# Performance work log

Hardware: AMD Instinct MI355X
Metric: run time of the kernel (lower is better)

Reference implementation:

```python
import jax, jax.numpy as jnp
import numpy as np

N_NODES = 50000
N_EDGES = 800000
D_IN = 128
D_OUT = 128


def setup_inputs() -> dict:
    key = jax.random.key(0)
    k1, k2, k3, k4, k5 = jax.random.split(key, 5)
    x = jax.random.normal(k1, (N_NODES, D_IN), dtype=jnp.float32)
    # fc weight, torch Linear convention: [out_dim, in_dim]
    W = jax.random.normal(k2, (D_OUT, D_IN), dtype=jnp.float32) * (1.0 / np.sqrt(D_IN))
    # attn_fc weight: [1, 2*out_dim], no bias
    a = jax.random.normal(k3, (1, 2 * D_OUT), dtype=jnp.float32) * (1.0 / np.sqrt(2 * D_OUT))
    src = jax.random.randint(k4, (N_EDGES,), 0, N_NODES)
    dst = jax.random.randint(k5, (N_EDGES,), 0, N_NODES)
    return {"x": x, "W": W, "a": a, "src": src, "dst": dst}


def reference(x, W, a, src, dst):
    # h = fc(x)
    h = x @ W.T  # [N, D_OUT]
    # attn_fc(cat([h_src, h_dst])) == h_src @ a[:D] + h_dst @ a[D:] (linear, no bias),
    # so precompute per-node scalars instead of materializing [E, 2*D_OUT].
    a_src = a[0, :D_OUT]
    a_dst = a[0, D_OUT:]
    s = h @ a_src  # [N]
    d = h @ a_dst  # [N]
    e = jax.nn.sigmoid(s[src] + d[dst])[:, None]  # [E, 1]
    msg = e * h[src]  # [E, D_OUT]  edge gather + weight
    # reduce: f[v] = sum over incoming edges of e * h_src
    f = jax.ops.segment_sum(msg, dst, num_segments=N_NODES)  # [N, D_OUT]
    return f
```

## Files before the change

kernel.cpp:

```cpp
#include <hip/hip_runtime.h>
#include <hip/hip_bf16.h>
#include <stdint.h>

#define NN 50000
#define NE 800000
#define DD 128
#define NBKT 782
#define BCH 4096
#define BGRID ((NE + BCH - 1) / BCH)
#define CAP 1280
#define SPILL_CAP 32768
#define GROWS 32
#define GGRID ((NN + GROWS - 1) / GROWS)

typedef __attribute__((ext_vector_type(8))) unsigned short ushort8;
typedef __attribute__((ext_vector_type(8))) short short8;
typedef __attribute__((ext_vector_type(4))) float f32x4;

__device__ inline uint16_t f2bf(float f) {
    uint32_t u = __float_as_uint(f);
    return (uint16_t)((u + 0x7fffu + ((u >> 16) & 1u)) >> 16);
}
__device__ inline float bf_lo(uint32_t u) { return __uint_as_float(u << 16); }
__device__ inline float bf_hi(uint32_t u) { return __uint_as_float(u & 0xffff0000u); }

__global__ __launch_bounds__(256) void wconv_k(const float* __restrict__ W,
                                               uint16_t* __restrict__ Wb,
                                               int* __restrict__ cntg) {
    int t = threadIdx.x;
    if (blockIdx.x == 0) {
        for (int k = t; k < NBKT + 4; k += 256) cntg[k] = 0;
    }
    int i = blockIdx.x * 256 + t;
    if (i < DD * DD) Wb[i] = f2bf(W[i]);
}

__global__ __launch_bounds__(256) void gemm_mfma_k(const float* __restrict__ x,
                                                   const uint16_t* __restrict__ Wb,
                                                   const float* __restrict__ a,
                                                   uint16_t* __restrict__ hb,
                                                   float* __restrict__ sArr,
                                                   float* __restrict__ dArr) {
    __shared__ __align__(16) uint16_t hs[GROWS][136];
    __shared__ float sdl[2 * GROWS];
    const int t = threadIdx.x, l = t & 63, wid = t >> 6;
    const int r0 = blockIdx.x * GROWS;
    const int wr0 = (wid >> 1) * 16;
    const int wc0 = (wid & 1) * 64;
    const int lr = l & 15, lk = l >> 4;
    if (t < 2 * GROWS) sdl[t] = 0.f;
    __syncthreads();

    f32x4 acc[4] = {{0.f,0.f,0.f,0.f},{0.f,0.f,0.f,0.f},{0.f,0.f,0.f,0.f},{0.f,0.f,0.f,0.f}};
    const int arow = r0 + wr0 + lr;
    const bool rok = arow < NN;
    const float* xp = x + (size_t)arow * DD + lk * 8;

    #pragma unroll
    for (int kc = 0; kc < 4; ++kc) {
        short8 af;
        if (rok) {
            float4 v0 = *(const float4*)(xp + kc * 32);
            float4 v1 = *(const float4*)(xp + kc * 32 + 4);
            af[0] = (short)f2bf(v0.x); af[1] = (short)f2bf(v0.y);
            af[2] = (short)f2bf(v0.z); af[3] = (short)f2bf(v0.w);
            af[4] = (short)f2bf(v1.x); af[5] = (short)f2bf(v1.y);
            af[6] = (short)f2bf(v1.z); af[7] = (short)f2bf(v1.w);
        } else {
            af = short8{0,0,0,0,0,0,0,0};
        }
        #pragma unroll
        for (int c = 0; c < 4; ++c) {
            int col = wc0 + c * 16 + lr;
            short8 bf_ = *(const short8*)(Wb + (size_t)col * DD + kc * 32 + lk * 8);
            acc[c] = __builtin_amdgcn_mfma_f32_16x16x32_bf16(af, bf_, acc[c], 0, 0, 0);
        }
    }

    float avs[4], avd[4];
    #pragma unroll
    for (int c = 0; c < 4; ++c) {
        avs[c] = a[wc0 + c * 16 + lr];
        avd[c] = a[DD + wc0 + c * 16 + lr];
    }
    #pragma unroll
    for (int i = 0; i < 4; ++i) {
        float ps = 0.f, pd = 0.f;
        #pragma unroll
        for (int c = 0; c < 4; ++c) {
            ps = fmaf(acc[c][i], avs[c], ps);
            pd = fmaf(acc[c][i], avd[c], pd);
        }
        #pragma unroll
        for (int o = 8; o > 0; o >>= 1) {
            ps += __shfl_xor(ps, o);
            pd += __shfl_xor(pd, o);
        }
        if (lr == 0) {
            int brow = wr0 + lk * 4 + i;
            atomicAdd(&sdl[brow], ps);
            atomicAdd(&sdl[GROWS + brow], pd);
        }
    }
    #pragma unroll
    for (int c = 0; c < 4; ++c)
        #pragma unroll
        for (int i = 0; i < 4; ++i)
            hs[wr0 + lk * 4 + i][wc0 + c * 16 + lr] = f2bf(acc[c][i]);
    __syncthreads();

    {
        int row = t >> 3, colg = (t & 7) * 16;
        int grow = r0 + row;
        if (grow < NN) {
            ushort8 v0 = *(const ushort8*)&hs[row][colg];
            ushort8 v1 = *(const ushort8*)&hs[row][colg + 8];
            *(ushort8*)(hb + (size_t)grow * DD + colg) = v0;
            *(ushort8*)(hb + (size_t)grow * DD + colg + 8) = v1;
        }
    }
    if (t < GROWS) {
        int grow = r0 + t;
        if (grow < NN) { sArr[grow] = sdl[t]; dArr[grow] = sdl[GROWS + t]; }
    }
}

__global__ __launch_bounds__(256) void bscat_k(const int* __restrict__ src,
                                               const int* __restrict__ dst,
                                               int* __restrict__ cntg,
                                               int* __restrict__ spill_cnt,
                                               uint32_t* __restrict__ rec,
                                               uint2* __restrict__ spill) {
    __shared__ int lh[NBKT];
    __shared__ int gb[NBKT];
    int t = threadIdx.x;
    for (int k = t; k < NBKT; k += 256) lh[k] = 0;
    __syncthreads();
    int base = blockIdx.x * BCH;
    unsigned pk[16]; int bk[16];
    #pragma unroll
    for (int i = 0; i < 16; ++i) {
        int idx = base + i * 256 + t;
        if (idx < NE) {
            int s_ = src[idx], d_ = dst[idx];
            bk[i] = d_ >> 6;
            pk[i] = ((unsigned)(d_ & 63) << 16) | (unsigned)s_;
            atomicAdd(&lh[bk[i]], 1);
        } else bk[i] = -1;
    }
    __syncthreads();
    for (int k = t; k < NBKT; k += 256) {
        int c = lh[k];
        lh[k] = 0;
        if (c) gb[k] = atomicAdd(&cntg[k], c);
    }
    __syncthreads();
    #pragma unroll
    for (int i = 0; i < 16; ++i) {
        if (bk[i] >= 0) {
            int sl = atomicAdd(&lh[bk[i]], 1);
            int p = gb[bk[i]] + sl;
            if (p < CAP) {
                rec[(size_t)bk[i] * CAP + p] = pk[i];
            } else {
                int sp = atomicAdd(spill_cnt, 1);
                if (sp < SPILL_CAP)
                    spill[sp] = make_uint2(pk[i] & 0xffffu,
                                           (unsigned)(bk[i] * 64 + (int)(pk[i] >> 16)));
            }
        }
    }
}

__global__ __launch_bounds__(512) void bsort_agg_k(const uint32_t* __restrict__ hb,
                                                   const float* __restrict__ sA,
                                                   const float* __restrict__ dA,
                                                   const int* __restrict__ cntg,
                                                   const uint32_t* __restrict__ rec,
                                                   float* __restrict__ out) {
    __shared__ uint32_t srt[CAP];
    __shared__ float    eL[CAP];
    __shared__ float dAl[64];
    __shared__ int h64[64];
    __shared__ int s65[65];
    __shared__ int curw[64];
    int t = threadIdx.x, l = t & 63, wid = t >> 6;
    int b = blockIdx.x;
    int cnt = cntg[b]; if (cnt > CAP) cnt = CAP;
    int beg = b * CAP;
    int n0 = b * 64;
    if (t < 64) {
        h64[t] = 0;
        int n = n0 + t;
        dAl[t] = (n < NN) ? dA[n] : 0.f;
    }
    __syncthreads();

    uint32_t rc[3]; int nrc = 0;
    for (int j = t; j < cnt; j += 512) {
        uint32_t r = rec[beg + j];
        rc[nrc++] = r;
        atomicAdd(&h64[r >> 16], 1);
    }
    __syncthreads();
    if (wid == 0) {
        int v = h64[l];
        int inc = v;
        #pragma unroll
        for (int o = 1; o < 64; o <<= 1) {
            int nb = __shfl_up(inc, o);
            if (l >= o) inc += nb;
        }
        s65[l + 1] = inc;
        if (l == 0) s65[0] = 0;
        curw[l] = inc - v;
    }
    __syncthreads();
    for (int k = 0; k < nrc; ++k) {
        uint32_t r = rc[k];
        int d = (int)(r >> 16);
        int p = atomicAdd(&curw[d], 1);
        float z = sA[r & 0xffffu] + dAl[d];
        srt[p] = r;
        eL[p] = 1.f / (1.f + __expf(-z));
    }
    __syncthreads();
    #pragma unroll 1
    for (int rr = 0; rr < 8; ++rr) {
        int d = wid * 8 + rr;
        int n = n0 + d;
        if (n >= NN) break;
        int js = s65[d], je = s65[d + 1];
        float2 a0 = {0.f,0.f}, a1 = {0.f,0.f}, a2 = {0.f,0.f}, a3 = {0.f,0.f};
        int j = js;
        for (; j + 3 < je; j += 4) {
            uint32_t r0 = srt[j], r1 = srt[j+1], r2 = srt[j+2], r3 = srt[j+3];
            float e0 = eL[j], e1 = eL[j+1], e2 = eL[j+2], e3 = eL[j+3];
            uint32_t u0 = hb[(size_t)(r0 & 0xffffu) * 64 + l];
            uint32_t u1 = hb[(size_t)(r1 & 0xffffu) * 64 + l];
            uint32_t u2 = hb[(size_t)(r2 & 0xffffu) * 64 + l];
            uint32_t u3 = hb[(size_t)(r3 & 0xffffu) * 64 + l];
            a0.x = fmaf(e0, bf_lo(u0), a0.x); a0.y = fmaf(e0, bf_hi(u0), a0.y);
            a1.x = fmaf(e1, bf_lo(u1), a1.x); a1.y = fmaf(e1, bf_hi(u1), a1.y);
            a2.x = fmaf(e2, bf_lo(u2), a2.x); a2.y = fmaf(e2, bf_hi(u2), a2.y);
            a3.x = fmaf(e3, bf_lo(u3), a3.x); a3.y = fmaf(e3, bf_hi(u3), a3.y);
        }
        for (; j < je; ++j) {
            uint32_t r0 = srt[j];
            float e0 = eL[j];
            uint32_t u0 = hb[(size_t)(r0 & 0xffffu) * 64 + l];
            a0.x = fmaf(e0, bf_lo(u0), a0.x); a0.y = fmaf(e0, bf_hi(u0), a0.y);
        }
        float2 res;
        res.x = (a0.x + a1.x) + (a2.x + a3.x);
        res.y = (a0.y + a1.y) + (a2.y + a3.y);
        ((float2*)out)[(size_t)n * 64 + l] = res;
    }
}

__global__ __launch_bounds__(256) void spill_k(const int* __restrict__ spill_cnt,
                                               const uint2* __restrict__ spill,
                                               const float* __restrict__ sA,
                                               const float* __restrict__ dA,
                                               const uint32_t* __restrict__ hb,
                                               float* __restrict__ out) {
    int n = *spill_cnt; if (n > SPILL_CAP) n = SPILL_CAP;
    int w = blockIdx.x * 4 + (threadIdx.x >> 6), l = threadIdx.x & 63;
    for (int i = w; i < n; i += 32) {
        uint2 r = spill[i];
        float z = sA[r.x] + dA[r.y];
        float e = 1.f / (1.f + __expf(-z));
        uint32_t u = hb[(size_t)r.x * 64 + l];
        atomicAdd(&out[(size_t)r.y * DD + 2 * l],     e * bf_lo(u));
        atomicAdd(&out[(size_t)r.y * DD + 2 * l + 1], e * bf_hi(u));
    }
}

__global__ __launch_bounds__(256) void edge_atomic_k(const int* __restrict__ src, const int* __restrict__ dst,
                                                     const float* __restrict__ sArr, const float* __restrict__ dArr,
                                                     const uint32_t* __restrict__ hb, float* __restrict__ out) {
    int wid = threadIdx.x >> 6, l = threadIdx.x & 63;
    int e = blockIdx.x * 4 + wid;
    if (e >= NE) return;
    int sv = src[e], dv = dst[e];
    float z = sArr[sv] + dArr[dv];
    float ev = 1.0f / (1.0f + __expf(-z));
    uint32_t u = hb[(size_t)sv * 64 + l];
    atomicAdd(&out[(size_t)dv * DD + 2 * l],     ev * bf_lo(u));
    atomicAdd(&out[(size_t)dv * DD + 2 * l + 1], ev * bf_hi(u));
}

extern "C" void kernel_launch(void* const* d_in, const int* in_sizes, int n_in,
                              void* d_out, int out_size, void* d_ws, size_t ws_size,
                              hipStream_t stream) {
    const float* x  = (const float*)d_in[0];
    const float* W  = (const float*)d_in[1];
    const float* a  = (const float*)d_in[2];
    const int* src  = (const int*)d_in[3];
    const int* dst  = (const int*)d_in[4];
    float* out = (float*)d_out;

    char* p = (char*)d_ws;
    uint16_t* hb = (uint16_t*)p;            p += (size_t)NN * DD * 2;
    uint16_t* Wb = (uint16_t*)p;            p += (size_t)DD * DD * 2;
    float* sA    = (float*)p;               p += (size_t)NN * 4;
    float* dA    = (float*)p;               p += (size_t)NN * 4;
    int*   cntg  = (int*)p;                 p += (size_t)NBKT * 4;
    int*   scnt  = (int*)p;                 p += 16;
    uint32_t* rec = (uint32_t*)(((uintptr_t)p + 15) & ~(uintptr_t)15);
    p = (char*)(rec + (size_t)NBKT * CAP);
    uint2* spill = (uint2*)p;               p += (size_t)SPILL_CAP * 8;
    size_t need  = (size_t)(p - (char*)d_ws);

    if (ws_size >= need) {
        wconv_k<<<64, 256, 0, stream>>>(W, Wb, cntg);
        gemm_mfma_k<<<GGRID, 256, 0, stream>>>(x, Wb, a, hb, sA, dA);
        bscat_k<<<BGRID, 256, 0, stream>>>(src, dst, cntg, scnt, rec, spill);
        bsort_agg_k<<<NBKT, 512, 0, stream>>>((const uint32_t*)hb, sA, dA, cntg, rec, out);
        spill_k<<<8, 256, 0, stream>>>(scnt, spill, sA, dA, (const uint32_t*)hb, out);
    } else {
        hipMemsetAsync(out, 0, sizeof(float) * (size_t)NN * DD, stream);
        wconv_k<<<64, 256, 0, stream>>>(W, Wb, cntg);
        gemm_mfma_k<<<GGRID, 256, 0, stream>>>(x, Wb, a, hb, sA, dA);
        edge_atomic_k<<<NE / 4, 256, 0, stream>>>(src, dst, sA, dA, (const uint32_t*)hb, out);
    }
}
```

Baseline: 85.92 us.

## Widen GEMM tile per wave, shrink scatter chunks, unroll gather by eight

The GEMM kernel now has each wave compute all 128 output columns for 16 rows, with 64 rows per block. Because each wave holds full rows, the s/d attention scalars are written straight to global memory, removing the shared-memory atomics and the extra barrier. The bucket scatter halves its per-block chunk to launch more blocks with fewer registers per thread. The aggregation loop adds an 8-way unrolled gather to keep more independent loads in flight, at the cost of higher register pressure.

```diff
diff --git a/kernel.cpp b/kernel.cpp
--- a/kernel.cpp
+++ b/kernel.cpp
@@ -6,11 +6,11 @@
 #define NE 800000
 #define DD 128
 #define NBKT 782
-#define BCH 4096
+#define BCH 2048
 #define BGRID ((NE + BCH - 1) / BCH)
 #define CAP 1280
 #define SPILL_CAP 32768
-#define GROWS 32
+#define GROWS 64
 #define GGRID ((NN + GROWS - 1) / GROWS)
 
 typedef __attribute__((ext_vector_type(8))) unsigned short ushort8;
@@ -42,17 +42,15 @@
                                                    float* __restrict__ sArr,
                                                    float* __restrict__ dArr) {
     __shared__ __align__(16) uint16_t hs[GROWS][136];
-    __shared__ float sdl[2 * GROWS];
     const int t = threadIdx.x, l = t & 63, wid = t >> 6;
     const int r0 = blockIdx.x * GROWS;
-    const int wr0 = (wid >> 1) * 16;
-    const int wc0 = (wid & 1) * 64;
     const int lr = l & 15, lk = l >> 4;
-    if (t < 2 * GROWS) sdl[t] = 0.f;
-    __syncthreads();
-
-    f32x4 acc[4] = {{0.f,0.f,0.f,0.f},{0.f,0.f,0.f,0.f},{0.f,0.f,0.f,0.f},{0.f,0.f,0.f,0.f}};
-    const int arow = r0 + wr0 + lr;
+
+    f32x4 acc[8];
+    #pragma unroll
+    for (int c = 0; c < 8; ++c) acc[c] = f32x4{0.f, 0.f, 0.f, 0.f};
+
+    const int arow = r0 + wid * 16 + lr;
     const bool rok = arow < NN;
     const float* xp = x + (size_t)arow * DD + lk * 8;
 
@@ -70,24 +68,24 @@
             af = short8{0,0,0,0,0,0,0,0};
         }
         #pragma unroll
-        for (int c = 0; c < 4; ++c) {
-            int col = wc0 + c * 16 + lr;
+        for (int c = 0; c < 8; ++c) {
+            int col = c * 16 + lr;
             short8 bf_ = *(const short8*)(Wb + (size_t)col * DD + kc * 32 + lk * 8);
             acc[c] = __builtin_amdgcn_mfma_f32_16x16x32_bf16(af, bf_, acc[c], 0, 0, 0);
         }
     }
 
-    float avs[4], avd[4];
-    #pragma unroll
-    for (int c = 0; c < 4; ++c) {
-        avs[c] = a[wc0 + c * 16 + lr];
-        avd[c] = a[DD + wc0 + c * 16 + lr];
+    float avs[8], avd[8];
+    #pragma unroll
+    for (int c = 0; c < 8; ++c) {
+        avs[c] = a[c * 16 + lr];
+        avd[c] = a[DD + c * 16 + lr];
     }
     #pragma unroll
     for (int i = 0; i < 4; ++i) {
         float ps = 0.f, pd = 0.f;
         #pragma unroll
-        for (int c = 0; c < 4; ++c) {
+        for (int c = 0; c < 8; ++c) {
             ps = fmaf(acc[c][i], avs[c], ps);
             pd = fmaf(acc[c][i], avd[c], pd);
         }
@@ -97,31 +95,27 @@
             pd += __shfl_xor(pd, o);
         }
         if (lr == 0) {
-            int brow = wr0 + lk * 4 + i;
-            atomicAdd(&sdl[brow], ps);
-            atomicAdd(&sdl[GROWS + brow], pd);
-        }
-    }
-    #pragma unroll
-    for (int c = 0; c < 4; ++c)
+            int row = r0 + wid * 16 + lk * 4 + i;
+            if (row < NN) { sArr[row] = ps; dArr[row] = pd; }
+        }
+    }
+    #pragma unroll
+    for (int c = 0; c < 8; ++c)
         #pragma unroll
         for (int i = 0; i < 4; ++i)
-            hs[wr0 + lk * 4 + i][wc0 + c * 16 + lr] = f2bf(acc[c][i]);
+            hs[wid * 16 + lk * 4 + i][c * 16 + lr] = f2bf(acc[c][i]);
     __syncthreads();
 
     {
-        int row = t >> 3, colg = (t & 7) * 16;
+        int row = t >> 2, cb = (t & 3) * 32;
         int grow = r0 + row;
         if (grow < NN) {
-            ushort8 v0 = *(const ushort8*)&hs[row][colg];
-            ushort8 v1 = *(const ushort8*)&hs[row][colg + 8];
-            *(ushort8*)(hb + (size_t)grow * DD + colg) = v0;
-            *(ushort8*)(hb + (size_t)grow * DD + colg + 8) = v1;
-        }
-    }
-    if (t < GROWS) {
-        int grow = r0 + t;
-        if (grow < NN) { sArr[grow] = sdl[t]; dArr[grow] = sdl[GROWS + t]; }
+            #pragma unroll
+            for (int k = 0; k < 4; ++k) {
+                ushort8 v = *(const ushort8*)&hs[row][cb + k * 8];
+                *(ushort8*)(hb + (size_t)grow * DD + cb + k * 8) = v;
+            }
+        }
     }
 }
 
@@ -137,9 +131,9 @@
     for (int k = t; k < NBKT; k += 256) lh[k] = 0;
     __syncthreads();
     int base = blockIdx.x * BCH;
-    unsigned pk[16]; int bk[16];
-    #pragma unroll
-    for (int i = 0; i < 16; ++i) {
+    unsigned pk[8]; int bk[8];
+    #pragma unroll
+    for (int i = 0; i < 8; ++i) {
         int idx = base + i * 256 + t;
         if (idx < NE) {
             int s_ = src[idx], d_ = dst[idx];
@@ -156,7 +150,7 @@
     }
     __syncthreads();
     #pragma unroll
-    for (int i = 0; i < 16; ++i) {
+    for (int i = 0; i < 8; ++i) {
         if (bk[i] >= 0) {
             int sl = atomicAdd(&lh[bk[i]], 1);
             int p = gb[bk[i]] + sl;
@@ -233,6 +227,28 @@
         int js = s65[d], je = s65[d + 1];
         float2 a0 = {0.f,0.f}, a1 = {0.f,0.f}, a2 = {0.f,0.f}, a3 = {0.f,0.f};
         int j = js;
+        for (; j + 7 < je; j += 8) {
+            uint32_t r0 = srt[j],   r1 = srt[j+1], r2 = srt[j+2], r3 = srt[j+3];
+            uint32_t r4 = srt[j+4], r5 = srt[j+5], r6 = srt[j+6], r7 = srt[j+7];
+            uint32_t u0 = hb[(size_t)(r0 & 0xffffu) * 64 + l];
+            uint32_t u1 = hb[(size_t)(r1 & 0xffffu) * 64 + l];
+            uint32_t u2 = hb[(size_t)(r2 & 0xffffu) * 64 + l];
+            uint32_t u3 = hb[(size_t)(r3 & 0xffffu) * 64 + l];
+            uint32_t u4 = hb[(size_t)(r4 & 0xffffu) * 64 + l];
+            uint32_t u5 = hb[(size_t)(r5 & 0xffffu) * 64 + l];
+            uint32_t u6 = hb[(size_t)(r6 & 0xffffu) * 64 + l];
+            uint32_t u7 = hb[(size_t)(r7 & 0xffffu) * 64 + l];
+            float e0 = eL[j],   e1 = eL[j+1], e2 = eL[j+2], e3 = eL[j+3];
+            float e4 = eL[j+4], e5 = eL[j+5], e6 = eL[j+6], e7 = eL[j+7];
+            a0.x = fmaf(e0, bf_lo(u0), a0.x); a0.y = fmaf(e0, bf_hi(u0), a0.y);
+            a1.x = fmaf(e1, bf_lo(u1), a1.x); a1.y = fmaf(e1, bf_hi(u1), a1.y);
+            a2.x = fmaf(e2, bf_lo(u2), a2.x); a2.y = fmaf(e2, bf_hi(u2), a2.y);
+            a3.x = fmaf(e3, bf_lo(u3), a3.x); a3.y = fmaf(e3, bf_hi(u3), a3.y);
+            a0.x = fmaf(e4, bf_lo(u4), a0.x); a0.y = fmaf(e4, bf_hi(u4), a0.y);
+            a1.x = fmaf(e5, bf_lo(u5), a1.x); a1.y = fmaf(e5, bf_hi(u5), a1.y);
+            a2.x = fmaf(e6, bf_lo(u6), a2.x); a2.y = fmaf(e6, bf_hi(u6), a2.y);
+            a3.x = fmaf(e7, bf_lo(u7), a3.x); a3.y = fmaf(e7, bf_hi(u7), a3.y);
+        }
         for (; j + 3 < je; j += 4) {
             uint32_t r0 = srt[j], r1 = srt[j+1], r2 = srt[j+2], r3 = srt[j+3];
             float e0 = eL[j], e1 = eL[j+1], e2 = eL[j+2], e3 = eL[j+3];
```

Result: slower. 87.64 us (+2.0%).
